# Kernel tuning notes

Measured on AMD Instinct MI355X. Metric: run time of the kernel, lower is better.

Reference implementation:

```python
import jax, jax.numpy as jnp
import numpy as np

L, H, N = 4096, 256, 64  # seq_len, hidden_size, hippo_n
EPS = 1e-5


def setup_inputs() -> dict:
    key = jax.random.key(0)
    ks = jax.random.split(key, 8)
    x = jax.random.normal(ks[0], (L, H), jnp.float32)
    # S4D-Lin style initialization for the diagonal SSM (H independent SSMs of state size N)
    Lambda_re = -0.5 * jnp.ones((H, N), jnp.float32)
    Lambda_im = jnp.tile(jnp.pi * jnp.arange(N, dtype=jnp.float32), (H, 1))
    B_re = jnp.ones((H, N), jnp.float32)
    B_im = jnp.zeros((H, N), jnp.float32)
    C_re = jax.random.normal(ks[1], (H, N), jnp.float32) * (0.5 ** 0.5)
    C_im = jax.random.normal(ks[2], (H, N), jnp.float32) * (0.5 ** 0.5)
    D = jax.random.normal(ks[3], (H,), jnp.float32)
    log_step = jax.random.uniform(ks[4], (H,), jnp.float32,
                                  minval=jnp.log(0.001), maxval=jnp.log(0.1))
    ln_w = jnp.ones((H,), jnp.float32)
    ln_b = jnp.zeros((H,), jnp.float32)
    sc = 1.0 / jnp.sqrt(jnp.float32(H))
    W1 = jax.random.normal(ks[5], (H, H), jnp.float32) * sc
    b1 = jnp.zeros((H,), jnp.float32)
    W2 = jax.random.normal(ks[6], (H, H), jnp.float32) * sc
    b2 = jnp.zeros((H,), jnp.float32)
    return {"x": x, "Lambda_re": Lambda_re, "Lambda_im": Lambda_im,
            "B_re": B_re, "B_im": B_im, "C_re": C_re, "C_im": C_im,
            "D": D, "log_step": log_step, "ln_w": ln_w, "ln_b": ln_b,
            "W1": W1, "b1": b1, "W2": W2, "b2": b2}


def reference(x, Lambda_re, Lambda_im, B_re, B_im, C_re, C_im, D, log_step,
              ln_w, ln_b, W1, b1, W2, b2):
    skip = x
    # per-token LayerNorm over the H feature axis (eqx.nn.LayerNorm, eps=1e-5)
    mu = jnp.mean(x, axis=-1, keepdims=True)
    var = jnp.mean(jnp.square(x - mu), axis=-1, keepdims=True)
    xn = (x - mu) / jnp.sqrt(var + EPS) * ln_w + ln_b  # [L, H]

    # ZOH discretization of the diagonal SSM (the cell.ssm(L) step)
    Lam = Lambda_re + 1j * Lambda_im                     # [H, N] complex64
    dt = jnp.exp(log_step)[:, None]                      # [H, 1]
    Ab = jnp.exp(Lam * dt)                               # [H, N]
    Bb = (Ab - 1.0) / Lam * (B_re + 1j * B_im)           # [H, N]
    C = C_re + 1j * C_im                                 # [H, N]

    def step(s, u):  # s: [H, N] complex state, u: [H] input at one time step
        s = Ab * s + Bb * u[:, None]
        y = 2.0 * jnp.einsum('hn,hn->h', C, s).real + D * u
        return s, y

    s0 = jnp.zeros((H, N), jnp.complex64)
    hidden, ys = jax.lax.scan(step, s0, xn)              # ys: [L, H]

    g = jax.nn.gelu(ys)
    out = (g @ W1.T + b1) * jax.nn.sigmoid(g @ W2.T + b2)  # GLU epilogue
    return (hidden, skip + out)
```

## Files before the change

kernel.cpp:

```cpp
#include <hip/hip_runtime.h>
#include <hip/hip_bf16.h>

#define LSEQ 4096
#define HDIM 256
#define NS   64
#define PC   32
#define MC   128

typedef __attribute__((ext_vector_type(8))) short short8;
typedef __attribute__((ext_vector_type(4))) float floatx4;

__device__ __forceinline__ float lane_bcast(float v, int j) {
    return __uint_as_float(__builtin_amdgcn_readlane(__float_as_uint(v), j));
}

__global__ __launch_bounds__(256) void k_pre(const float* __restrict__ x,
                                             const float* __restrict__ lnw,
                                             const float* __restrict__ lnb,
                                             const float* __restrict__ W1,
                                             const float* __restrict__ W2,
                                             float* __restrict__ xnT,
                                             unsigned short* __restrict__ w1b,
                                             unsigned short* __restrict__ w2b) {
    int t = threadIdx.x;
    if (blockIdx.x >= 256) {
        int g = (blockIdx.x - 256) * 256 + t;
        float4 a = ((const float4*)W1)[g];
        float4 c = ((const float4*)W2)[g];
        ushort4 o1, o2;
        __hip_bfloat16 hh;
        hh = __float2bfloat16(a.x); o1.x = *(unsigned short*)&hh;
        hh = __float2bfloat16(a.y); o1.y = *(unsigned short*)&hh;
        hh = __float2bfloat16(a.z); o1.z = *(unsigned short*)&hh;
        hh = __float2bfloat16(a.w); o1.w = *(unsigned short*)&hh;
        hh = __float2bfloat16(c.x); o2.x = *(unsigned short*)&hh;
        hh = __float2bfloat16(c.y); o2.y = *(unsigned short*)&hh;
        hh = __float2bfloat16(c.z); o2.z = *(unsigned short*)&hh;
        hh = __float2bfloat16(c.w); o2.w = *(unsigned short*)&hh;
        ((ushort4*)w1b)[g] = o1;
        ((ushort4*)w2b)[g] = o2;
        return;
    }
    __shared__ float tile[16][257];
    __shared__ float smu[16], srs[16];
    int l0 = blockIdx.x * 16;
#pragma unroll
    for (int i = 0; i < 16; ++i)
        tile[i][t] = x[(size_t)(l0 + i) * HDIM + t];
    __syncthreads();
    int wv = t >> 6, lane = t & 63;
#pragma unroll
    for (int k = 0; k < 4; ++k) {
        int i = wv * 4 + k;
        float s = 0.f, s2 = 0.f;
#pragma unroll
        for (int q = 0; q < 4; ++q) {
            float v = tile[i][lane + 64 * q];
            s += v; s2 += v * v;
        }
#pragma unroll
        for (int o = 32; o; o >>= 1) {
            s  += __shfl_xor(s, o);
            s2 += __shfl_xor(s2, o);
        }
        if (lane == 0) {
            float m = s * (1.0f / HDIM);
            smu[i] = m;
            srs[i] = rsqrtf(s2 * (1.0f / HDIM) - m * m + 1e-5f);
        }
    }
    __syncthreads();
    float wh = lnw[t], bh = lnb[t];
    float o[16];
#pragma unroll
    for (int i = 0; i < 16; ++i)
        o[i] = (tile[i][t] - smu[i]) * srs[i] * wh + bh;
    float4* dst = (float4*)(xnT + (size_t)t * LSEQ + l0);
#pragma unroll
    for (int k = 0; k < 4; ++k)
        dst[k] = make_float4(o[4 * k], o[4 * k + 1], o[4 * k + 2], o[4 * k + 3]);
}

__device__ inline void ssm_consts(const float* Lre, const float* Lim,
                                  const float* Bre, const float* Bim,
                                  const float* lstep, int h, int n,
                                  float& are, float& aim, float& bre, float& bim) {
    int idx = h * NS + n;
    float lre = Lre[idx], lim = Lim[idx];
    float dt = expf(lstep[h]);
    float er = expf(lre * dt);
    float sa, ca;
    sincosf(lim * dt, &sa, &ca);
    are = er * ca; aim = er * sa;
    float inv = 1.0f / (lre * lre + lim * lim);
    float nre = are - 1.0f, nim = aim;
    float tre = (nre * lre + nim * lim) * inv;
    float tim = (nim * lre - nre * lim) * inv;
    float br = Bre[idx], bi = Bim[idx];
    bre = tre * br - tim * bi;
    bim = tre * bi + tim * br;
}

__global__ __launch_bounds__(1024) void k_scan(const float* __restrict__ xnT,
                                               const float* __restrict__ Lre,
                                               const float* __restrict__ Lim,
                                               const float* __restrict__ Bre,
                                               const float* __restrict__ Bim,
                                               const float* __restrict__ Cre,
                                               const float* __restrict__ Cim,
                                               const float* __restrict__ Dv,
                                               const float* __restrict__ lstep,
                                               __hip_bfloat16* __restrict__ gb,
                                               float* __restrict__ hid,
                                               int interleaved) {
    __shared__ float2 fst[PC * NS];
    __shared__ __align__(16) float red[16][8 * 68];
    int h = blockIdx.x;
    int wv = __builtin_amdgcn_readfirstlane((int)threadIdx.x) >> 6;
    int lane = threadIdx.x & 63, n = lane;
    const float* uh = xnT + (size_t)h * LSEQ;

    float are, aim, bre, bim;
    ssm_consts(Lre, Lim, Bre, Bim, lstep, h, n, are, aim, bre, bim);
    int idx = h * NS + n;
    float cre = Cre[idx], cim = Cim[idx];
    float Dh = Dv[h];

#pragma unroll
    for (int cc = 0; cc < 2; ++cc) {
        int c = wv * 2 + cc;
        const float* u = uh + c * MC;
        float sre = 0.f, sim = 0.f;
        for (int g = 0; g < 2; ++g) {
            float uv = u[g * 64 + lane];
#pragma unroll
            for (int j = 0; j < 64; ++j) {
                float us = lane_bcast(uv, j);
                float nr = fmaf(are, sre, fmaf(-aim, sim, bre * us));
                float ni = fmaf(are, sim, fmaf( aim, sre, bim * us));
                sre = nr; sim = ni;
            }
        }
        fst[c * NS + n] = make_float2(sre, sim);
    }
    __syncthreads();

    if (wv == 0) {
        float ar = are, ai = aim;
#pragma unroll
        for (int q = 0; q < 7; ++q) {
            float r2 = ar * ar - ai * ai;
            ai = 2.f * ar * ai;
            ar = r2;
        }
        float sre = 0.f, sim = 0.f;
        for (int c = 0; c < PC; ++c) {
            float2 fc = fst[c * NS + n];
            fst[c * NS + n] = make_float2(sre, sim);
            float nr = fmaf(ar, sre, fmaf(-ai, sim, fc.x));
            float ni = fmaf(ar, sim, fmaf( ai, sre, fc.y));
            sre = nr; sim = ni;
        }
        if (interleaved) {
            ((float2*)hid)[idx] = make_float2(sre, sim);
        } else {
            hid[idx] = sre;
        }
    }
    __syncthreads();

    float* rw = red[wv];
    int t8 = lane & 7, p = lane >> 3;
#pragma unroll
    for (int cc = 0; cc < 2; ++cc) {
        int c = wv * 2 + cc;
        const float* u = uh + c * MC;
        float2 s00 = fst[c * NS + n];
        float sre = s00.x, sim = s00.y;
        for (int g = 0; g < 2; ++g) {
            float uv = u[g * 64 + lane];
#pragma unroll
            for (int jg = 0; jg < 8; ++jg) {
#pragma unroll
                for (int tt = 0; tt < 8; ++tt) {
                    float us = lane_bcast(uv, jg * 8 + tt);
                    float nr = fmaf(are, sre, fmaf(-aim, sim, bre * us));
                    float ni = fmaf(are, sim, fmaf( aim, sre, bim * us));
                    sre = nr; sim = ni;
                    rw[tt * 68 + n] = fmaf(cre, sre, -(cim * sim));
                }
                const float4* rp = (const float4*)(rw + t8 * 68 + p * 8);
                float4 v0 = rp[0], v1 = rp[1];
                float a0 = ((v0.x + v0.y) + (v0.z + v0.w)) +
                           ((v1.x + v1.y) + (v1.z + v1.w));
                a0 += __shfl_xor(a0, 8);
                a0 += __shfl_xor(a0, 16);
                a0 += __shfl_xor(a0, 32);
                float u_tok = __shfl(uv, jg * 8 + t8);
                if (lane < 8) {
                    int l = c * MC + g * 64 + jg * 8 + t8;
                    float y = fmaf(2.f, a0, Dh * u_tok);
                    float z = 0.7978845608028654f * fmaf(0.044715f, y * y * y, y);
                    float e = __expf(2.f * z);
                    float th = 1.f - 2.f / (e + 1.f);
                    float gg = 0.5f * y * (1.f + th);
                    gb[(size_t)l * HDIM + h] = __float2bfloat16(gg);
                }
            }
        }
    }
}

__global__ __launch_bounds__(64) void k_glu_mfma(const unsigned short* __restrict__ gbs,
                                                 const unsigned short* __restrict__ w1b,
                                                 const unsigned short* __restrict__ w2b,
                                                 const float* __restrict__ b1v,
                                                 const float* __restrict__ b2v,
                                                 const float* __restrict__ x,
                                                 float* __restrict__ out) {
    int bx = blockIdx.x;
    int m0 = (bx >> 3) * 32;
    int n0 = (bx & 7) * 32;
    int lane = threadIdx.x;
    int t = lane & 15, q = lane >> 4;

    floatx4 acc[2][2][2];
#pragma unroll
    for (int a = 0; a < 2; ++a)
#pragma unroll
        for (int b = 0; b < 2; ++b)
#pragma unroll
            for (int g = 0; g < 2; ++g)
                acc[a][b][g] = (floatx4){0.f, 0.f, 0.f, 0.f};

    const unsigned short* A0  = gbs + (size_t)(m0 + t) * HDIM + q * 8;
    const unsigned short* A1  = A0 + 16 * HDIM;
    const unsigned short* B10 = w1b + (size_t)(n0 + t) * HDIM + q * 8;
    const unsigned short* B11 = B10 + 16 * HDIM;
    const unsigned short* B20 = w2b + (size_t)(n0 + t) * HDIM + q * 8;
    const unsigned short* B21 = B20 + 16 * HDIM;

#pragma unroll
    for (int ks = 0; ks < 8; ++ks) {
        int off = ks * 32;
        short8 a0  = *(const short8*)(A0  + off);
        short8 a1  = *(const short8*)(A1  + off);
        short8 b10 = *(const short8*)(B10 + off);
        short8 b11 = *(const short8*)(B11 + off);
        short8 b20 = *(const short8*)(B20 + off);
        short8 b21 = *(const short8*)(B21 + off);
        acc[0][0][0] = __builtin_amdgcn_mfma_f32_16x16x32_bf16(a0, b10, acc[0][0][0], 0, 0, 0);
        acc[0][1][0] = __builtin_amdgcn_mfma_f32_16x16x32_bf16(a0, b11, acc[0][1][0], 0, 0, 0);
        acc[1][0][0] = __builtin_amdgcn_mfma_f32_16x16x32_bf16(a1, b10, acc[1][0][0], 0, 0, 0);
        acc[1][1][0] = __builtin_amdgcn_mfma_f32_16x16x32_bf16(a1, b11, acc[1][1][0], 0, 0, 0);
        acc[0][0][1] = __builtin_amdgcn_mfma_f32_16x16x32_bf16(a0, b20, acc[0][0][1], 0, 0, 0);
        acc[0][1][1] = __builtin_amdgcn_mfma_f32_16x16x32_bf16(a0, b21, acc[0][1][1], 0, 0, 0);
        acc[1][0][1] = __builtin_amdgcn_mfma_f32_16x16x32_bf16(a1, b20, acc[1][0][1], 0, 0, 0);
        acc[1][1][1] = __builtin_amdgcn_mfma_f32_16x16x32_bf16(a1, b21, acc[1][1][1], 0, 0, 0);
    }

#pragma unroll
    for (int nt = 0; nt < 2; ++nt) {
        int hh = n0 + nt * 16 + t;
        float bb1 = b1v[hh], bb2 = b2v[hh];
#pragma unroll
        for (int mt = 0; mt < 2; ++mt) {
#pragma unroll
            for (int reg = 0; reg < 4; ++reg) {
                int l = m0 + mt * 16 + q * 4 + reg;
                float a  = acc[mt][nt][0][reg] + bb1;
                float sg = 1.f / (1.f + __expf(-(acc[mt][nt][1][reg] + bb2)));
                out[(size_t)l * HDIM + hh] = fmaf(a, sg, x[(size_t)l * HDIM + hh]);
            }
        }
    }
}

extern "C" void kernel_launch(void* const* d_in, const int* in_sizes, int n_in,
                              void* d_out, int out_size, void* d_ws, size_t ws_size,
                              hipStream_t stream) {
    (void)in_sizes; (void)n_in; (void)ws_size;
    const float* x     = (const float*)d_in[0];
    const float* Lre   = (const float*)d_in[1];
    const float* Lim   = (const float*)d_in[2];
    const float* Bre   = (const float*)d_in[3];
    const float* Bim   = (const float*)d_in[4];
    const float* Cre   = (const float*)d_in[5];
    const float* Cim   = (const float*)d_in[6];
    const float* Dv    = (const float*)d_in[7];
    const float* lstep = (const float*)d_in[8];
    const float* lnw   = (const float*)d_in[9];
    const float* lnb   = (const float*)d_in[10];
    const float* W1    = (const float*)d_in[11];
    const float* b1    = (const float*)d_in[12];
    const float* W2    = (const float*)d_in[13];
    const float* b2    = (const float*)d_in[14];

    float* ws   = (float*)d_ws;
    float* xnT  = ws;
    unsigned short* gb  = (unsigned short*)(xnT + (size_t)HDIM * LSEQ);
    unsigned short* w1b = gb + (size_t)LSEQ * HDIM;
    unsigned short* w2b = w1b + HDIM * HDIM;

    int interleaved = (out_size == LSEQ * HDIM + 2 * HDIM * NS) ? 1 : 0;
    float* hid  = (float*)d_out;
    float* outp = (float*)d_out + (interleaved ? 2 * HDIM * NS : HDIM * NS);

    k_pre      <<<256 + 64, 256, 0, stream>>>(x, lnw, lnb, W1, W2, xnT, w1b, w2b);
    k_scan     <<<HDIM, 1024, 0, stream>>>(xnT, Lre, Lim, Bre, Bim, Cre, Cim,
                                           Dv, lstep, (__hip_bfloat16*)gb, hid, interleaved);
    k_glu_mfma <<<128 * 8, 64, 0, stream>>>(gb, w1b, w2b, b1, b2, x, outp);
}
```

Before: 135.9 us.

## Recast per-head SSM scan as chunked bf16 MFMA matmuls with Toeplitz kernel

Replaces the sequential per-token complex recurrence in k_scan with a chunked formulation. Within each 128-token chunk, the output comes from a lower-triangular Toeplitz matrix of the SSM convolution kernel applied to the inputs. The chunk-final states and the state-to-output contributions are likewise computed as bf16 MFMA matmuls, with only a short 32-step inter-chunk recurrence left sequential. The block shrinks from 1024 to 256 threads and uses about 60KB of LDS. The risk is accuracy loss from bf16 quantization of the inputs, kernel and states.

```diff
diff --git a/kernel.cpp b/kernel.cpp
--- a/kernel.cpp
+++ b/kernel.cpp
@@ -10,8 +10,17 @@
 typedef __attribute__((ext_vector_type(8))) short short8;
 typedef __attribute__((ext_vector_type(4))) float floatx4;
 
-__device__ __forceinline__ float lane_bcast(float v, int j) {
-    return __uint_as_float(__builtin_amdgcn_readlane(__float_as_uint(v), j));
+__device__ __forceinline__ short b16(float x) {
+    __hip_bfloat16 h = __float2bfloat16(x);
+    return *(reinterpret_cast<short*>(&h));
+}
+__device__ __forceinline__ unsigned int pk2(float a, float b) {
+    return (unsigned int)(unsigned short)b16(a) | ((unsigned int)(unsigned short)b16(b) << 16);
+}
+__device__ __forceinline__ void cmul(float& xr, float& xi, float yr, float yi) {
+    float r = xr * yr - xi * yi;
+    float i = xr * yi + xi * yr;
+    xr = r; xi = i;
 }
 
 __global__ __launch_bounds__(256) void k_pre(const float* __restrict__ x,
@@ -28,15 +37,10 @@
         float4 a = ((const float4*)W1)[g];
         float4 c = ((const float4*)W2)[g];
         ushort4 o1, o2;
-        __hip_bfloat16 hh;
-        hh = __float2bfloat16(a.x); o1.x = *(unsigned short*)&hh;
-        hh = __float2bfloat16(a.y); o1.y = *(unsigned short*)&hh;
-        hh = __float2bfloat16(a.z); o1.z = *(unsigned short*)&hh;
-        hh = __float2bfloat16(a.w); o1.w = *(unsigned short*)&hh;
-        hh = __float2bfloat16(c.x); o2.x = *(unsigned short*)&hh;
-        hh = __float2bfloat16(c.y); o2.y = *(unsigned short*)&hh;
-        hh = __float2bfloat16(c.z); o2.z = *(unsigned short*)&hh;
-        hh = __float2bfloat16(c.w); o2.w = *(unsigned short*)&hh;
+        o1.x = (unsigned short)b16(a.x); o1.y = (unsigned short)b16(a.y);
+        o1.z = (unsigned short)b16(a.z); o1.w = (unsigned short)b16(a.w);
+        o2.x = (unsigned short)b16(c.x); o2.y = (unsigned short)b16(c.y);
+        o2.z = (unsigned short)b16(c.z); o2.w = (unsigned short)b16(c.w);
         ((ushort4*)w1b)[g] = o1;
         ((ushort4*)w2b)[g] = o2;
         return;
@@ -81,13 +85,11 @@
         dst[k] = make_float4(o[4 * k], o[4 * k + 1], o[4 * k + 2], o[4 * k + 3]);
 }
 
-__device__ inline void ssm_consts(const float* Lre, const float* Lim,
-                                  const float* Bre, const float* Bim,
-                                  const float* lstep, int h, int n,
-                                  float& are, float& aim, float& bre, float& bim) {
-    int idx = h * NS + n;
+__device__ __forceinline__ void ssm_consts(const float* Lre, const float* Lim,
+                                           const float* Bre, const float* Bim,
+                                           float dt, int idx,
+                                           float& are, float& aim, float& bre, float& bim) {
     float lre = Lre[idx], lim = Lim[idx];
-    float dt = expf(lstep[h]);
     float er = expf(lre * dt);
     float sa, ca;
     sincosf(lim * dt, &sa, &ca);
@@ -101,111 +103,217 @@
     bim = tre * bi + tim * br;
 }
 
-__global__ __launch_bounds__(1024) void k_scan(const float* __restrict__ xnT,
-                                               const float* __restrict__ Lre,
-                                               const float* __restrict__ Lim,
-                                               const float* __restrict__ Bre,
-                                               const float* __restrict__ Bim,
-                                               const float* __restrict__ Cre,
-                                               const float* __restrict__ Cim,
-                                               const float* __restrict__ Dv,
-                                               const float* __restrict__ lstep,
-                                               __hip_bfloat16* __restrict__ gb,
-                                               float* __restrict__ hid,
-                                               int interleaved) {
-    __shared__ float2 fst[PC * NS];
-    __shared__ __align__(16) float red[16][8 * 68];
+__global__ __launch_bounds__(256) void k_scan(const float* __restrict__ xnT,
+                                              const float* __restrict__ Lre,
+                                              const float* __restrict__ Lim,
+                                              const float* __restrict__ Bre,
+                                              const float* __restrict__ Bim,
+                                              const float* __restrict__ Cre,
+                                              const float* __restrict__ Cim,
+                                              const float* __restrict__ Dv,
+                                              const float* __restrict__ lstep,
+                                              __hip_bfloat16* __restrict__ gb,
+                                              float* __restrict__ hid,
+                                              int interleaved) {
+    __shared__ __align__(16) unsigned char ldsb[60672];
+    short* ubf = (short*)(ldsb);
+    short* Tm  = (short*)(ldsb + 8704);
+    float* Ff  = (float*)(ldsb + 43520);
+    short* S0s = (short*)(ldsb + 43520);
+    float* Kt  = (float*)(ldsb + 60160);
+
     int h = blockIdx.x;
-    int wv = __builtin_amdgcn_readfirstlane((int)threadIdx.x) >> 6;
-    int lane = threadIdx.x & 63, n = lane;
+    int tid = threadIdx.x;
+    int wv = __builtin_amdgcn_readfirstlane(tid) >> 6;
+    int lane = tid & 63;
+    int l15 = lane & 15, q = lane >> 4;
     const float* uh = xnT + (size_t)h * LSEQ;
 
+    float dt = expf(lstep[h]);
+    float Dh = Dv[h];
+
     float are, aim, bre, bim;
-    ssm_consts(Lre, Lim, Bre, Bim, lstep, h, n, are, aim, bre, bim);
-    int idx = h * NS + n;
-    float cre = Cre[idx], cim = Cim[idx];
-    float Dh = Dv[h];
-
-#pragma unroll
-    for (int cc = 0; cc < 2; ++cc) {
-        int c = wv * 2 + cc;
-        const float* u = uh + c * MC;
-        float sre = 0.f, sim = 0.f;
-        for (int g = 0; g < 2; ++g) {
-            float uv = u[g * 64 + lane];
-#pragma unroll
-            for (int j = 0; j < 64; ++j) {
-                float us = lane_bcast(uv, j);
-                float nr = fmaf(are, sre, fmaf(-aim, sim, bre * us));
-                float ni = fmaf(are, sim, fmaf( aim, sre, bim * us));
-                sre = nr; sim = ni;
+    ssm_consts(Lre, Lim, Bre, Bim, dt, h * NS + lane, are, aim, bre, bim);
+    float cre = Cre[h * NS + lane], cim = Cim[h * NS + lane];
+
+    float A8r = are, A8i = aim;
+    cmul(A8r, A8i, A8r, A8i); cmul(A8r, A8i, A8r, A8i); cmul(A8r, A8i, A8r, A8i);
+    float A16r = A8r, A16i = A8i;  cmul(A16r, A16i, A16r, A16i);
+    float A32r = A16r, A32i = A16i; cmul(A32r, A32i, A32r, A32i);
+    float A64r = A32r, A64i = A32i; cmul(A64r, A64i, A64r, A64i);
+
+#pragma unroll
+    for (int k = 0; k < 4; ++k) {
+        int i4 = k * 1024 + tid * 4;
+        float4 v = *(const float4*)(uh + i4);
+        int c = i4 >> 7, col = i4 & 127;
+        unsigned int* d = (unsigned int*)(ubf + c * 136 + col);
+        d[0] = pk2(v.x, v.y);
+        d[1] = pk2(v.z, v.w);
+    }
+
+    {
+        float cbre = cre * bre - cim * bim;
+        float cbim = cre * bim + cim * bre;
+        float pr = 1.f, pi = 0.f;
+        if (wv & 1) cmul(pr, pi, A32r, A32i);
+        if (wv & 2) cmul(pr, pi, A64r, A64i);
+        for (int i = 0; i < 32; ++i) {
+            float kj = 2.f * (cbre * pr - cbim * pi);
+#pragma unroll
+            for (int o = 1; o <= 32; o <<= 1) kj += __shfl_xor(kj, o);
+            if (lane == 0) Kt[32 * wv + i] = kj;
+            cmul(pr, pi, are, aim);
+        }
+    }
+    __syncthreads();
+
+#pragma unroll 4
+    for (int it = 0; it < 64; ++it) {
+        int idx = it * 256 + tid;
+        int row = idx >> 7, col = idx & 127;
+        float kv = Kt[(row - col) & 127];
+        Tm[row * 136 + col] = (col <= row) ? b16(kv) : (short)0;
+    }
+
+    {
+        int n2 = 16 * wv + l15;
+        float are2, aim2, bre2, bim2;
+        ssm_consts(Lre, Lim, Bre, Bim, dt, h * NS + n2, are2, aim2, bre2, bim2);
+        float B8r = are2, B8i = aim2;
+        cmul(B8r, B8i, B8r, B8i); cmul(B8r, B8i, B8r, B8i); cmul(B8r, B8i, B8r, B8i);
+        float B16r = B8r, B16i = B8i;  cmul(B16r, B16i, B16r, B16i);
+        float B32r = B16r, B32i = B16i; cmul(B32r, B32i, B32r, B32i);
+        float B64r = B32r, B64i = B32i; cmul(B64r, B64i, B64r, B64i);
+
+        floatx4 fR[2], fI[2];
+#pragma unroll
+        for (int nt = 0; nt < 2; ++nt) { fR[nt] = (floatx4){0,0,0,0}; fI[nt] = (floatx4){0,0,0,0}; }
+
+#pragma unroll
+        for (int ks = 0; ks < 4; ++ks) {
+            int m8 = 15 - 4 * ks - q;
+            float sR = 1.f, sI = 0.f, tR, tI;
+            tR = sR * B8r - sI * B8i;  tI = sR * B8i + sI * B8r;
+            sR = (m8 & 1) ? tR : sR;   sI = (m8 & 1) ? tI : sI;
+            tR = sR * B16r - sI * B16i; tI = sR * B16i + sI * B16r;
+            sR = (m8 & 2) ? tR : sR;   sI = (m8 & 2) ? tI : sI;
+            tR = sR * B32r - sI * B32i; tI = sR * B32i + sI * B32r;
+            sR = (m8 & 4) ? tR : sR;   sI = (m8 & 4) ? tI : sI;
+            tR = sR * B64r - sI * B64i; tI = sR * B64i + sI * B64r;
+            sR = (m8 & 8) ? tR : sR;   sI = (m8 & 8) ? tI : sI;
+            short8 aR, aI;
+            float curR = sR, curI = sI;
+#pragma unroll
+            for (int e = 7; e >= 0; --e) {
+                aR[e] = b16(bre2 * curR - bim2 * curI);
+                aI[e] = b16(bre2 * curI + bim2 * curR);
+                if (e) cmul(curR, curI, are2, aim2);
             }
-        }
-        fst[c * NS + n] = make_float2(sre, sim);
+#pragma unroll
+            for (int nt = 0; nt < 2; ++nt) {
+                short8 bf = *(short8*)(ubf + (16 * nt + l15) * 136 + 32 * ks + 8 * q);
+                fR[nt] = __builtin_amdgcn_mfma_f32_16x16x32_bf16(aR, bf, fR[nt], 0, 0, 0);
+                fI[nt] = __builtin_amdgcn_mfma_f32_16x16x32_bf16(aI, bf, fI[nt], 0, 0, 0);
+            }
+        }
+#pragma unroll
+        for (int nt = 0; nt < 2; ++nt) {
+            int c = 16 * nt + l15;
+            float* fp = Ff + c * 130;
+#pragma unroll
+            for (int reg = 0; reg < 4; ++reg) {
+                int ns = 16 * wv + q * 4 + reg;
+                fp[ns]      = fR[nt][reg];
+                fp[65 + ns] = fI[nt][reg];
+            }
+        }
     }
     __syncthreads();
 
     if (wv == 0) {
-        float ar = are, ai = aim;
-#pragma unroll
-        for (int q = 0; q < 7; ++q) {
-            float r2 = ar * ar - ai * ai;
-            ai = 2.f * ar * ai;
-            ar = r2;
-        }
+        float a128r = A64r, a128i = A64i;
+        cmul(a128r, a128i, A64r, A64i);
         float sre = 0.f, sim = 0.f;
         for (int c = 0; c < PC; ++c) {
-            float2 fc = fst[c * NS + n];
-            fst[c * NS + n] = make_float2(sre, sim);
-            float nr = fmaf(ar, sre, fmaf(-ai, sim, fc.x));
-            float ni = fmaf(ar, sim, fmaf( ai, sre, fc.y));
+            float fre = Ff[c * 130 + lane];
+            float fim = Ff[c * 130 + 65 + lane];
+            ((unsigned int*)(ldsb + 43520 + 272 * c))[lane] = pk2(sre, sim);
+            float nr = fmaf(a128r, sre, fmaf(-a128i, sim, fre));
+            float ni = fmaf(a128r, sim, fmaf( a128i, sre, fim));
             sre = nr; sim = ni;
         }
         if (interleaved) {
-            ((float2*)hid)[idx] = make_float2(sre, sim);
+            ((float2*)hid)[h * NS + lane] = make_float2(sre, sim);
         } else {
-            hid[idx] = sre;
-        }
-    }
-    __syncthreads();
-
-    float* rw = red[wv];
-    int t8 = lane & 7, p = lane >> 3;
-#pragma unroll
-    for (int cc = 0; cc < 2; ++cc) {
-        int c = wv * 2 + cc;
-        const float* u = uh + c * MC;
-        float2 s00 = fst[c * NS + n];
-        float sre = s00.x, sim = s00.y;
-        for (int g = 0; g < 2; ++g) {
-            float uv = u[g * 64 + lane];
-#pragma unroll
-            for (int jg = 0; jg < 8; ++jg) {
-#pragma unroll
-                for (int tt = 0; tt < 8; ++tt) {
-                    float us = lane_bcast(uv, jg * 8 + tt);
-                    float nr = fmaf(are, sre, fmaf(-aim, sim, bre * us));
-                    float ni = fmaf(are, sim, fmaf( aim, sre, bim * us));
-                    sre = nr; sim = ni;
-                    rw[tt * 68 + n] = fmaf(cre, sre, -(cim * sim));
-                }
-                const float4* rp = (const float4*)(rw + t8 * 68 + p * 8);
-                float4 v0 = rp[0], v1 = rp[1];
-                float a0 = ((v0.x + v0.y) + (v0.z + v0.w)) +
-                           ((v1.x + v1.y) + (v1.z + v1.w));
-                a0 += __shfl_xor(a0, 8);
-                a0 += __shfl_xor(a0, 16);
-                a0 += __shfl_xor(a0, 32);
-                float u_tok = __shfl(uv, jg * 8 + t8);
-                if (lane < 8) {
-                    int l = c * MC + g * 64 + jg * 8 + t8;
-                    float y = fmaf(2.f, a0, Dh * u_tok);
-                    float z = 0.7978845608028654f * fmaf(0.044715f, y * y * y, y);
-                    float e = __expf(2.f * z);
-                    float th = 1.f - 2.f / (e + 1.f);
-                    float gg = 0.5f * y * (1.f + th);
-                    gb[(size_t)l * HDIM + h] = __float2bfloat16(gg);
-                }
+            hid[h * NS + lane] = sre;
+        }
+    }
+
+    floatx4 Y[2][2];
+#pragma unroll
+    for (int mi = 0; mi < 2; ++mi)
+#pragma unroll
+        for (int nt = 0; nt < 2; ++nt) Y[mi][nt] = (floatx4){0, 0, 0, 0};
+
+#pragma unroll
+    for (int ks = 0; ks < 4; ++ks) {
+        short8 bf0 = *(short8*)(ubf + l15 * 136 + 32 * ks + 8 * q);
+        short8 bf1 = *(short8*)(ubf + (16 + l15) * 136 + 32 * ks + 8 * q);
+#pragma unroll
+        for (int mi = 0; mi < 2; ++mi) {
+            int row = 16 * (2 * wv + mi) + l15;
+            short8 ta = *(short8*)(Tm + row * 136 + 32 * ks + 8 * q);
+            Y[mi][0] = __builtin_amdgcn_mfma_f32_16x16x32_bf16(ta, bf0, Y[mi][0], 0, 0, 0);
+            Y[mi][1] = __builtin_amdgcn_mfma_f32_16x16x32_bf16(ta, bf1, Y[mi][1], 0, 0, 0);
+        }
+    }
+    __syncthreads();
+
+    {
+        float pr = 1.f, pi = 0.f;
+        if (wv & 1) cmul(pr, pi, A32r, A32i);
+        if (wv & 2) cmul(pr, pi, A64r, A64i);
+        cmul(pr, pi, are, aim);
+        for (int i = 0; i < 32; ++i) {
+            int t = 32 * wv + i;
+            float er =  2.f * (cre * pr - cim * pi);
+            float en = -2.f * (cre * pi + cim * pr);
+            ((unsigned int*)(ldsb + 8704 + 272 * t))[lane] = pk2(er, en);
+            cmul(pr, pi, are, aim);
+        }
+    }
+    __syncthreads();
+
+#pragma unroll
+    for (int ks = 0; ks < 4; ++ks) {
+        short8 sf0 = *(short8*)(S0s + l15 * 136 + 32 * ks + 8 * q);
+        short8 sf1 = *(short8*)(S0s + (16 + l15) * 136 + 32 * ks + 8 * q);
+#pragma unroll
+        for (int mi = 0; mi < 2; ++mi) {
+            int row = 16 * (2 * wv + mi) + l15;
+            short8 ea = *(short8*)(Tm + row * 136 + 32 * ks + 8 * q);
+            Y[mi][0] = __builtin_amdgcn_mfma_f32_16x16x32_bf16(ea, sf0, Y[mi][0], 0, 0, 0);
+            Y[mi][1] = __builtin_amdgcn_mfma_f32_16x16x32_bf16(ea, sf1, Y[mi][1], 0, 0, 0);
+        }
+    }
+
+#pragma unroll
+    for (int mi = 0; mi < 2; ++mi) {
+#pragma unroll
+        for (int nt = 0; nt < 2; ++nt) {
+#pragma unroll
+            for (int reg = 0; reg < 4; ++reg) {
+                int t = 16 * (2 * wv + mi) + q * 4 + reg;
+                int c = 16 * nt + l15;
+                int l = c * MC + t;
+                float u = uh[l];
+                float y = Y[mi][nt][reg] + Dh * u;
+                float z = 0.7978845608028654f * fmaf(0.044715f, y * y * y, y);
+                float e = __expf(2.f * z);
+                float th = 1.f - 2.f / (e + 1.f);
+                float gg = 0.5f * y * (1.f + th);
+                gb[((size_t)l << 8) + h] = __float2bfloat16(gg);
             }
         }
     }
@@ -307,7 +415,7 @@
     float* outp = (float*)d_out + (interleaved ? 2 * HDIM * NS : HDIM * NS);
 
     k_pre      <<<256 + 64, 256, 0, stream>>>(x, lnw, lnb, W1, W2, xnT, w1b, w2b);
-    k_scan     <<<HDIM, 1024, 0, stream>>>(xnT, Lre, Lim, Bre, Bim, Cre, Cim,
-                                           Dv, lstep, (__hip_bfloat16*)gb, hid, interleaved);
+    k_scan     <<<HDIM, 256, 0, stream>>>(xnT, Lre, Lim, Bre, Bim, Cre, Cim,
+                                          Dv, lstep, (__hip_bfloat16*)gb, hid, interleaved);
     k_glu_mfma <<<128 * 8, 64, 0, stream>>>(gb, w1b, w2b, b1, b2, x, outp);
 }
```

Result: faster. 122.9 us (-9.6%).
